# Optimization experiments

Hardware: AMD Instinct MI355X
Metric: run time of the kernel (lower is better)

The kernel has to match this reference:

```python
import jax, jax.numpy as jnp
import numpy as np
import math

N, E, LAT, MUL, HD = 20000, 160000, 128, 16, 32
H = LAT // HD          # 4 heads
D = 9                  # 0e+1o+2e spherical harmonics dim
SLICES = ((0, 1), (1, 4), (4, 9))
TPD = MUL * len(SLICES)


def _mlp(x, W1, b1, W2, b2):
    return jnp.dot(jax.nn.silu(jnp.dot(x, W1) + b1), W2) + b2


def _eq_linear(x, W):
    # block-diagonal per-l channel mixing: x [E, mul, D], W [n_l, mul, mul]
    return jnp.concatenate([jnp.einsum('ji,eim->ejm', W[l], x[:, :, s:t])
                            for l, (s, t) in enumerate(SLICES)], axis=-1)


def _residual(x, x_new, uc):
    co = jax.lax.rsqrt(uc * uc + 1.0)
    return co * x + (uc * co) * x_new


def _vec_rej(feat, dirs):
    d = dirs[:, None, :]
    return feat - (feat * d).sum(-1, keepdims=True) * d


def _so3_ln(x, eps=1e-8):
    # equivariant RMS layernorm per irrep block
    out = []
    for s, t in SLICES:
        blk = x[:, :, s:t]
        rms = jnp.sqrt((blk * blk).sum(-1).mean(-1) + eps)  # [N]
        out.append(blk / rms[:, None, None])
    return jnp.concatenate(out, axis=-1)


def _ln(x, g, b, eps=1e-5):
    mu = x.mean(-1, keepdims=True)
    var = ((x - mu) ** 2).mean(-1, keepdims=True)
    return (x - mu) * jax.lax.rsqrt(var + eps) * g + b


def _forward(h, X, t_ij, spharms, update_coeff, Wtq, Wtk, Wrs_W, Wrs_b, Wq_W, Wq_b, Wk_W, Wk_b, Wre_W, ln_g, ln_b, Wvu,
             gs_W1, gs_b1, gs_W2, gs_b2, gv_W1, gv_b1, gv_W2, gv_b2, gw_W1, gw_b1, gw_W2, gw_b2,
             gt_W1, gt_b1, gt_W2, gt_b2, gsp_W1, gsp_b1, gsp_W2, gsp_b2, md_W1, md_b1, md_W2, md_b2,
             mt_W1, mt_b1, mt_W2, mt_b2, gm_W1, gm_b1, gm_W2, gm_b2,
             edge_center, edge_neighbor, num_nodes):
    uc = update_coeff
    Xn = X[edge_neighbor]                                     # [E, mul, D]
    Xq = _vec_rej(_eq_linear(X[edge_center], Wtq), spharms)
    Xk = _vec_rej(_eq_linear(Xn, Wtk), -spharms)
    # CG scalar contraction (l x l -> 0e, uuu): normalized per-l dot product
    w = jnp.concatenate([(Xq[:, :, s:t] * Xk[:, :, s:t]).sum(-1) / math.sqrt(t - s)
                         for s, t in SLICES], axis=-1)        # [E, 3*mul]
    dt = _mlp(w, gw_W1, gw_b1, gw_W2, gw_b2) * _mlp(t_ij, gt_W1, gt_b1, gt_W2, gt_b2)
    t_ij = _residual(t_ij, dt, uc)
    h_i = h[edge_center]
    h_j = h[edge_neighbor]
    spatial = (t_ij @ Wrs_W + Wrs_b) * _mlp(h_j, gs_W1, gs_b1, gs_W2, gs_b2)
    En = t_ij.shape[0]
    q = (h_i @ Wq_W + Wq_b).reshape(En, H, HD)
    k = (h_j @ Wk_W + Wk_b).reshape(En, H, HD)
    v = _mlp(h_j, gv_W1, gv_b1, gv_W2, gv_b2)
    ta = jax.nn.silu(t_ij @ Wre_W).reshape(En, H, HD)
    alpha = (q * k * ta).sum(-1) / math.sqrt(HD)              # [E, H]
    amax = jax.ops.segment_max(alpha, edge_center, num_segments=num_nodes)
    ex = jnp.exp(alpha - amax[edge_center])
    den = jax.ops.segment_sum(ex, edge_center, num_segments=num_nodes)
    attn = ex / den[edge_center]                              # scatter_softmax
    sea = (attn[:, :, None] * v.reshape(En, H, HD)).reshape(En, LAT)
    combined = sea + spatial
    gates = _mlp(combined, gsp_W1, gsp_b1, gsp_W2, gsp_b2)
    o_s, o_d, o_t = gates[:, :LAT], gates[:, LAT:2 * LAT], gates[:, 2 * LAT:]
    dh = _ln(jax.ops.segment_sum(o_s, edge_center, num_segments=num_nodes), ln_g, ln_b)
    h = _residual(h, dh, uc)
    gd = _mlp(o_d, md_W1, md_b1, md_W2, md_b2)
    gtt = _mlp(o_t, mt_W1, mt_b1, mt_W2, mt_b2)
    dXij = gd[:, :, None] * spharms[:, None, :] + gtt[:, :, None] * Xn
    dX = _so3_ln(jax.ops.segment_sum(dXij, edge_center, num_segments=num_nodes))
    X = _residual(X, dX, uc)
    # EQFF
    Xp = jnp.einsum('nmi,mj->nji', X, Wvu)
    nrm = jnp.sqrt((Xp * Xp).sum(-1) + 1e-12)
    g = _mlp(jnp.concatenate([h, nrm], axis=-1), gm_W1, gm_b1, gm_W2, gm_b2)
    h = h + g[:, :LAT]
    X = X + g[:, LAT:, None] * Xp
    return h, X, t_ij


def setup_inputs() -> dict:
    key = jax.random.key(0)
    ks = jax.random.split(key, 24)

    def mk_mlp(k, din, dout):
        k1, k2 = jax.random.split(k)
        return (jax.random.normal(k1, (din, LAT)) / math.sqrt(din), jnp.zeros((LAT,)),
                jax.random.normal(k2, (LAT, dout)) / math.sqrt(LAT), jnp.zeros((dout,)))

    inp = {
        'h': jax.random.normal(ks[0], (N, LAT)),
        'X': jax.random.normal(ks[1], (N, MUL, D)),
        't_ij': jax.random.normal(ks[2], (E, LAT)),
        'spharms': jax.random.normal(ks[3], (E, D)),
        'update_coeff': jnp.ones((1,), dtype=jnp.float32),
        'Wtq': jax.random.normal(ks[4], (len(SLICES), MUL, MUL)) / math.sqrt(MUL),
        'Wtk': jax.random.normal(ks[5], (len(SLICES), MUL, MUL)) / math.sqrt(MUL),
        'Wrs_W': jax.random.normal(ks[6], (LAT, LAT)) / math.sqrt(LAT),
        'Wrs_b': jnp.zeros((LAT,)),
        'Wq_W': jax.random.normal(ks[7], (LAT, LAT)) / math.sqrt(LAT),
        'Wq_b': jnp.zeros((LAT,)),
        'Wk_W': jax.random.normal(ks[8], (LAT, LAT)) / math.sqrt(LAT),
        'Wk_b': jnp.zeros((LAT,)),
        'Wre_W': jax.random.normal(ks[9], (LAT, LAT)) / math.sqrt(LAT),
        'ln_g': jnp.ones((LAT,)),
        'ln_b': jnp.zeros((LAT,)),
        'Wvu': jax.random.normal(ks[10], (MUL, MUL)) / math.sqrt(MUL),
    }
    for name, din, dout, k in [('gs', LAT, LAT, ks[11]), ('gv', LAT, LAT, ks[12]), ('gw', TPD, LAT, ks[13]),
                               ('gt', LAT, LAT, ks[14]), ('gsp', LAT, 3 * LAT, ks[15]), ('md', LAT, MUL, ks[16]),
                               ('mt', LAT, MUL, ks[17]), ('gm', LAT + MUL, LAT + MUL, ks[18])]:
        W1, b1, W2, b2 = mk_mlp(k, din, dout)
        inp[name + '_W1'], inp[name + '_b1'], inp[name + '_W2'], inp[name + '_b2'] = W1, b1, W2, b2
    inp['edge_center'] = jax.random.randint(ks[19], (E,), 0, N)
    inp['edge_neighbor'] = jax.random.randint(ks[20], (E,), 0, N)
    inp['num_nodes'] = N
    return inp


def reference(h, X, t_ij, spharms, update_coeff, Wtq, Wtk, Wrs_W, Wrs_b, Wq_W, Wq_b, Wk_W, Wk_b, Wre_W, ln_g, ln_b, Wvu,
              gs_W1, gs_b1, gs_W2, gs_b2, gv_W1, gv_b1, gv_W2, gv_b2, gw_W1, gw_b1, gw_W2, gw_b2,
              gt_W1, gt_b1, gt_W2, gt_b2, gsp_W1, gsp_b1, gsp_W2, gsp_b2, md_W1, md_b1, md_W2, md_b2,
              mt_W1, mt_b1, mt_W2, mt_b2, gm_W1, gm_b1, gm_W2, gm_b2,
              edge_center, edge_neighbor, num_nodes):
    return _forward(h, X, t_ij, spharms, update_coeff, Wtq, Wtk, Wrs_W, Wrs_b, Wq_W, Wq_b, Wk_W, Wk_b, Wre_W, ln_g, ln_b, Wvu,
                    gs_W1, gs_b1, gs_W2, gs_b2, gv_W1, gv_b1, gv_W2, gv_b2, gw_W1, gw_b1, gw_W2, gw_b2,
                    gt_W1, gt_b1, gt_W2, gt_b2, gsp_W1, gsp_b1, gsp_W2, gsp_b2, md_W1, md_b1, md_W2, md_b2,
                    mt_W1, mt_b1, mt_W2, mt_b2, gm_W1, gm_b1, gm_W2, gm_b2,
                    edge_center, edge_neighbor, num_nodes)
```

## Files before the change

### kernel.cpp

```cpp
#include <hip/hip_runtime.h>
#include <math.h>

#define N_NODES 20000
#define E_EDGES 160000
#define LAT 128
#define MUL 16
#define DD 9
#define TPD 48

#define WS_QB     ((size_t)0)
#define WS_KB     (WS_QB + (size_t)N_NODES*LAT/2)
#define WS_VB     (WS_KB + (size_t)N_NODES*LAT/2)
#define WS_SB     (WS_VB + (size_t)N_NODES*LAT/2)
#define WS_W48    (WS_SB + (size_t)N_NODES*LAT/2)
#define WS_SPATB  (WS_W48 + (size_t)E_EDGES*TPD)
#define WS_ALPHA  (WS_SPATB + (size_t)E_EDGES*LAT/2)
#define WS_ZERO   (WS_ALPHA + (size_t)E_EDGES*4)
#define WS_AMAX   WS_ZERO
#define WS_DEN    (WS_AMAX + (size_t)N_NODES*4)
#define WS_HSUM   (WS_DEN + (size_t)N_NODES*4)
#define WS_NDX    (WS_HSUM + (size_t)N_NODES*LAT/2)
#define WS_END    (WS_NDX + (size_t)N_NODES*72)
#define ZERO_CNT  (WS_END - WS_ZERO)
#define WS_WB     WS_END

#define WOFF_WQ   0
#define WOFF_WK   16384
#define WOFF_GV1  32768
#define WOFF_GV2  49152
#define WOFF_GS1  65536
#define WOFF_GS2  81920
#define WOFF_GW1  98304
#define WOFF_GW2  106496
#define WOFF_GT1  122880
#define WOFF_GT2  139264
#define WOFF_WRS  155648
#define WOFF_WRE  172032
#define WOFF_GSP1 188416
#define WOFF_GSP2 204800
#define WOFF_MD1  253952
#define WOFF_MD2  270336
#define WOFF_MT1  272384
#define WOFF_MT2  288768
#define WB_TOTAL  290816

#define DEVI __device__ __forceinline__

typedef short short8 __attribute__((ext_vector_type(8)));
typedef float f32x4 __attribute__((ext_vector_type(4)));

DEVI float silu_f(float x){ return x / (1.f + __expf(-x)); }
DEVI unsigned int fmap(float x){ unsigned int b=__float_as_uint(x); return (b&0x80000000u)? ~b : (b|0x80000000u); }
DEVI float funmap(unsigned int u){ return (u&0x80000000u)? __uint_as_float(u&0x7fffffffu) : __uint_as_float(~u); }

DEVI unsigned short f2b(float f){ unsigned int u=__float_as_uint(f); return (unsigned short)((u + 0x7fffu + ((u>>16)&1u))>>16); }
DEVI unsigned int f2b2(float lo, float hi){ return ((unsigned int)f2b(hi)<<16) | (unsigned int)f2b(lo); }
DEVI float b2f(unsigned short u){ return __uint_as_float(((unsigned int)u)<<16); }

DEVI void atom_pk(unsigned short* p, unsigned int pk){
  asm volatile("global_atomic_pk_add_bf16 %0, %1, off" :: "v"(p), "v"(pk) : "memory");
}

DEVI f32x4 mfma16(short8 a, short8 b, f32x4 c){
  return __builtin_amdgcn_mfma_f32_16x16x32_bf16(a,b,c,0,0,0);
}

template<int KB>
DEVI void mm_tile2(const unsigned short* act, int strideUS, const unsigned short* Wp,
                   int ntile, int m, int quad, f32x4* acc){
  const unsigned short* wp = Wp + (size_t)ntile*KB*512 + (size_t)quad*128 + m*8;
  const unsigned short* a0 = act + m*strideUS + quad*8;
  const unsigned short* a1 = a0 + 16*strideUS;
  #pragma unroll
  for (int kb=0;kb<KB;++kb){
    short8 bfr = *(const short8*)(wp + (size_t)kb*512);
    short8 af0 = *(const short8*)(a0 + kb*32);
    short8 af1 = *(const short8*)(a1 + kb*32);
    acc[0]=mfma16(af0,bfr,acc[0]);
    acc[1]=mfma16(af1,bfr,acc[1]);
  }
}

template<int KB>
DEVI void mm_tile1(const unsigned short* act, int strideUS, const unsigned short* Wp,
                   int mtbase, int m, int quad, f32x4& acc){
  const unsigned short* wp = Wp + (size_t)quad*128 + m*8;
  const unsigned short* a0 = act + (mtbase*16+m)*strideUS + quad*8;
  #pragma unroll
  for (int kb=0;kb<KB;++kb){
    short8 bfr = *(const short8*)(wp + (size_t)kb*512);
    short8 af  = *(const short8*)(a0 + kb*32);
    acc=mfma16(af,bfr,acc);
  }
}

template<int R, int KD, int LDSTRIDE>
DEVI void mm_acc(const float* src, const float* __restrict__ W, int wstride, int t, float* acc){
  #pragma unroll 2
  for (int k=0;k<KD;k+=4){
    float4 xv[R];
    #pragma unroll
    for (int r=0;r<R;++r) xv[r] = *(const float4*)(src + r*LDSTRIDE + k);
    #pragma unroll
    for (int kk=0;kk<4;++kk){
      float wk = W[(size_t)(k+kk)*wstride + t];
      #pragma unroll
      for (int r=0;r<R;++r) acc[r] += ((const float*)&xv[r])[kk]*wk;
    }
  }
}

__global__ void k0_zero(float* __restrict__ z){
  size_t i = (size_t)blockIdx.x*256 + threadIdx.x;
  if (i < ZERO_CNT) z[i] = 0.f;
}

__global__ __launch_bounds__(256) void k_pack(
  const float* __restrict__ Wq,const float* __restrict__ Wk,
  const float* __restrict__ gv1,const float* __restrict__ gv2,
  const float* __restrict__ gs1,const float* __restrict__ gs2,
  const float* __restrict__ gw1,const float* __restrict__ gw2,
  const float* __restrict__ gt1,const float* __restrict__ gt2,
  const float* __restrict__ Wrs,const float* __restrict__ Wre,
  const float* __restrict__ gsp1,const float* __restrict__ gsp2,
  const float* __restrict__ md1,const float* __restrict__ md2,
  const float* __restrict__ mt1,const float* __restrict__ mt2,
  unsigned short* __restrict__ dst)
{
  int i = blockIdx.x*256 + threadIdx.x;
  if (i >= WB_TOTAL) return;
  const int off[19] = {0,16384,32768,49152,65536,81920,98304,106496,122880,139264,
                       155648,172032,188416,204800,253952,270336,272384,288768,290816};
  int mi=0;
  while (i >= off[mi+1]) ++mi;
  int li = i - off[mi];
  int N = (mi==13)?384:((mi==15||mi==17)?16:128);
  int Ksrc = (mi==6)?48:128;
  int KB = (mi==6)?2:4;
  int j = li&7; int t = li>>3;
  int n_in = t&15; t>>=4;
  int quad = t&3; t>>=2;
  int k_block = t % KB; int n_tile = t / KB;
  int k = k_block*32 + quad*8 + j;
  int n = n_tile*16 + n_in;
  const float* src;
  switch(mi){
    case 0: src=Wq; break;  case 1: src=Wk; break;
    case 2: src=gv1; break; case 3: src=gv2; break;
    case 4: src=gs1; break; case 5: src=gs2; break;
    case 6: src=gw1; break; case 7: src=gw2; break;
    case 8: src=gt1; break; case 9: src=gt2; break;
    case 10: src=Wrs; break; case 11: src=Wre; break;
    case 12: src=gsp1; break; case 13: src=gsp2; break;
    case 14: src=md1; break; case 15: src=md2; break;
    default: src=(mi==16)?mt1:mt2; break;
  }
  float v = (k < Ksrc) ? src[(size_t)k*N + n] : 0.f;
  dst[i] = f2b(v);
}

__global__ __launch_bounds__(256) void k1_node(const float* __restrict__ h,
  const unsigned short* __restrict__ WB,
  const float* __restrict__ Wq_b,const float* __restrict__ Wk_b,
  const float* __restrict__ gv_b1,const float* __restrict__ gv_b2,
  const float* __restrict__ gs_b1,const float* __restrict__ gs_b2,
  float* __restrict__ ws)
{
  __shared__ __align__(16) unsigned short B0[32*136], B1[32*136];
  const int tid=threadIdx.x, lane=tid&63, w=tid>>6, m=lane&15, quad=lane>>4;
  const int n0=blockIdx.x*32;
  for (int idx=tid; idx<1024; idx+=256){ int r=idx>>5, c4=(idx&31)*4;
    float4 hv = *(const float4*)(h+(size_t)(n0+r)*128+c4);
    *(unsigned int*)(B0+r*136+c4)   = f2b2(hv.x,hv.y);
    *(unsigned int*)(B0+r*136+c4+2) = f2b2(hv.z,hv.w); }
  __syncthreads();
  unsigned short* Qb=(unsigned short*)(ws+WS_QB);
  unsigned short* Kb=(unsigned short*)(ws+WS_KB);
  unsigned short* Vb=(unsigned short*)(ws+WS_VB);
  unsigned short* Sb=(unsigned short*)(ws+WS_SB);
  f32x4 z4 = {0.f,0.f,0.f,0.f};
  { f32x4 acc[2][2]={{z4,z4},{z4,z4}};
    #pragma unroll
    for(int i=0;i<2;++i) mm_tile2<4>(B0,136,WB+WOFF_WQ, w*2+i, m, quad, acc[i]);
    #pragma unroll
    for(int i=0;i<2;++i){ int col=(w*2+i)*16+m; float bv=Wq_b[col];
      #pragma unroll
      for(int mt=0;mt<2;++mt)
        #pragma unroll
        for(int r=0;r<4;++r){ int row=mt*16+quad*4+r;
          Qb[(size_t)(n0+row)*128+col]=f2b(acc[i][mt][r]+bv); } } }
  { f32x4 acc[2][2]={{z4,z4},{z4,z4}};
    #pragma unroll
    for(int i=0;i<2;++i) mm_tile2<4>(B0,136,WB+WOFF_WK, w*2+i, m, quad, acc[i]);
    #pragma unroll
    for(int i=0;i<2;++i){ int col=(w*2+i)*16+m; float bv=Wk_b[col];
      #pragma unroll
      for(int mt=0;mt<2;++mt)
        #pragma unroll
        for(int r=0;r<4;++r){ int row=mt*16+quad*4+r;
          Kb[(size_t)(n0+row)*128+col]=f2b(acc[i][mt][r]+bv); } } }
  { f32x4 acc[2][2]={{z4,z4},{z4,z4}};
    #pragma unroll
    for(int i=0;i<2;++i) mm_tile2<4>(B0,136,WB+WOFF_GV1, w*2+i, m, quad, acc[i]);
    #pragma unroll
    for(int i=0;i<2;++i){ int col=(w*2+i)*16+m; float bv=gv_b1[col];
      #pragma unroll
      for(int mt=0;mt<2;++mt)
        #pragma unroll
        for(int r=0;r<4;++r) B1[(mt*16+quad*4+r)*136+col]=f2b(silu_f(acc[i][mt][r]+bv)); } }
  __syncthreads();
  { f32x4 acc[2][2]={{z4,z4},{z4,z4}};
    #pragma unroll
    for(int i=0;i<2;++i) mm_tile2<4>(B1,136,WB+WOFF_GV2, w*2+i, m, quad, acc[i]);
    #pragma unroll
    for(int i=0;i<2;++i){ int col=(w*2+i)*16+m; float bv=gv_b2[col];
      #pragma unroll
      for(int mt=0;mt<2;++mt)
        #pragma unroll
        for(int r=0;r<4;++r){ int row=mt*16+quad*4+r;
          Vb[(size_t)(n0+row)*128+col]=f2b(acc[i][mt][r]+bv); } } }
  __syncthreads();
  { f32x4 acc[2][2]={{z4,z4},{z4,z4}};
    #pragma unroll
    for(int i=0;i<2;++i) mm_tile2<4>(B0,136,WB+WOFF_GS1, w*2+i, m, quad, acc[i]);
    #pragma unroll
    for(int i=0;i<2;++i){ int col=(w*2+i)*16+m; float bv=gs_b1[col];
      #pragma unroll
      for(int mt=0;mt<2;++mt)
        #pragma unroll
        for(int r=0;r<4;++r) B1[(mt*16+quad*4+r)*136+col]=f2b(silu_f(acc[i][mt][r]+bv)); } }
  __syncthreads();
  { f32x4 acc[2][2]={{z4,z4},{z4,z4}};
    #pragma unroll
    for(int i=0;i<2;++i) mm_tile2<4>(B1,136,WB+WOFF_GS2, w*2+i, m, quad, acc[i]);
    #pragma unroll
    for(int i=0;i<2;++i){ int col=(w*2+i)*16+m; float bv=gs_b2[col];
      #pragma unroll
      for(int mt=0;mt<2;++mt)
        #pragma unroll
        for(int r=0;r<4;++r){ int row=mt*16+quad*4+r;
          Sb[(size_t)(n0+row)*128+col]=f2b(acc[i][mt][r]+bv); } } }
}

__global__ __launch_bounds__(256) void k2_edge_w(
  const float* __restrict__ Xin, const float* __restrict__ sph,
  const float* __restrict__ Wtq, const float* __restrict__ Wtk,
  const int* __restrict__ ec, const int* __restrict__ en, float* __restrict__ ws)
{
  __shared__ float xc[16][144], xn[16][144], sphL[16][9];
  __shared__ float wq[768], wkk[768];
  __shared__ int ceI[16], nbI[16];
  const int tid=threadIdx.x, e0=blockIdx.x*16;
  if (tid<16){ ceI[tid]=ec[e0+tid]; nbI[tid]=en[e0+tid]; }
  for (int idx=tid; idx<768; idx+=256){ wq[idx]=Wtq[idx]; wkk[idx]=Wtk[idx]; }
  __syncthreads();
  for (int idx=tid; idx<2304; idx+=256){ int r=idx/144,c=idx%144;
    xc[r][c]=Xin[(size_t)ceI[r]*144+c]; xn[r][c]=Xin[(size_t)nbI[r]*144+c]; }
  if (tid<144){ int r=tid/9,c=tid%9; sphL[r][c]=sph[(size_t)(e0+r)*9+c]; }
  __syncthreads();
  const int el=tid>>4, j=tid&15;
  float xq[9], xk[9];
  const int ss[3]={0,1,4}, se[3]={1,4,9};
  #pragma unroll
  for (int l=0;l<3;++l){
    for (int mm2=ss[l]; mm2<se[l]; ++mm2){
      float aq=0.f, ak=0.f;
      #pragma unroll
      for (int i=0;i<16;++i){
        float wql = wq[l*256 + j*16 + i], wkl = wkk[l*256 + j*16 + i];
        aq += wql*xc[el][i*9+mm2];
        ak += wkl*xn[el][i*9+mm2];
      }
      xq[mm2]=aq; xk[mm2]=ak;
    }
  }
  float dq=0.f, dk=0.f;
  #pragma unroll
  for (int d=0; d<9; ++d){ dq += xq[d]*sphL[el][d]; dk += xk[d]*sphL[el][d]; }
  #pragma unroll
  for (int d=0; d<9; ++d){ xq[d] -= dq*sphL[el][d]; xk[d] -= dk*sphL[el][d]; }
  const float isc[3] = {1.f, 0.5773502691896258f, 0.4472135954999579f};
  unsigned short* W48u = (unsigned short*)(ws+WS_W48);
  #pragma unroll
  for (int l=0;l<3;++l){
    float s=0.f;
    for (int mm2=ss[l]; mm2<se[l]; ++mm2) s += xq[mm2]*xk[mm2];
    W48u[(size_t)(e0+el)*TPD + l*16 + j] = f2b(s*isc[l]);
  }
}

__global__ __launch_bounds__(256) void k3_edge_t(
  const float* __restrict__ t_in, const int* __restrict__ ec, const int* __restrict__ en,
  const unsigned short* __restrict__ WB,
  const float* __restrict__ gw_b1,const float* __restrict__ gw_b2,
  const float* __restrict__ gt_b1,const float* __restrict__ gt_b2,
  const float* __restrict__ Wrs_b,
  const float* __restrict__ ucp, float* __restrict__ ws, float* __restrict__ outT)
{
  __shared__ __align__(16) unsigned short tin_b[32*136], hid_b[32*136];
  __shared__ int ceI[32], nbI[32];
  const int tid=threadIdx.x, lane=tid&63, w=tid>>6, m=lane&15, quad=lane>>4;
  const int e0=blockIdx.x*32;
  if (tid<32){ ceI[tid]=ec[e0+tid]; nbI[tid]=en[e0+tid]; }
  for (int idx=tid; idx<1024; idx+=256){ int r=idx>>5, c4=(idx&31)*4;
    float4 tv = *(const float4*)(t_in+(size_t)(e0+r)*128+c4);
    *(unsigned int*)(tin_b+r*136+c4)   = f2b2(tv.x,tv.y);
    *(unsigned int*)(tin_b+r*136+c4+2) = f2b2(tv.z,tv.w); }
  const unsigned short* W48u=(const unsigned short*)(ws+WS_W48);
  short8 wfr[2][2];
  #pragma unroll
  for (int rr=0;rr<2;++rr){
    const unsigned short* base = W48u + (size_t)(e0 + rr*16 + m)*TPD;
    wfr[rr][0] = *(const short8*)(base + quad*8);
    if (quad<2) wfr[rr][1] = *(const short8*)(base + 32 + quad*8);
    else { short8 z = {0,0,0,0,0,0,0,0}; wfr[rr][1] = z; }
  }
  __syncthreads();
  const float uc=ucp[0], co=rsqrtf(uc*uc+1.f), ucco=uc*co;
  f32x4 z4 = {0.f,0.f,0.f,0.f};
  { f32x4 acc[2][2]={{z4,z4},{z4,z4}};
    #pragma unroll
    for(int i=0;i<2;++i){
      const unsigned short* wp = WB+WOFF_GW1 + (size_t)(w*2+i)*1024 + (size_t)quad*128 + m*8;
      #pragma unroll
      for(int kb=0;kb<2;++kb){
        short8 bfr = *(const short8*)(wp + (size_t)kb*512);
        acc[i][0]=mfma16(wfr[0][kb],bfr,acc[i][0]);
        acc[i][1]=mfma16(wfr[1][kb],bfr,acc[i][1]);
      }
    }
    #pragma unroll
    for(int i=0;i<2;++i){ int col=(w*2+i)*16+m; float bv=gw_b1[col];
      #pragma unroll
      for(int mt=0;mt<2;++mt)
        #pragma unroll
        for(int r=0;r<4;++r) hid_b[(mt*16+quad*4+r)*136+col]=f2b(silu_f(acc[i][mt][r]+bv)); } }
  __syncthreads();
  f32x4 accw[2][2]={{z4,z4},{z4,z4}};
  #pragma unroll
  for(int i=0;i<2;++i) mm_tile2<4>(hid_b,136,WB+WOFF_GW2, w*2+i, m, quad, accw[i]);
// ... 25 lines not shown
  unsigned short* spatB = (unsigned short*)(ws+WS_SPATB);
  const unsigned short* Sb=(const unsigned short*)(ws+WS_SB);
  { f32x4 acc[2][2]={{z4,z4},{z4,z4}};
    #pragma unroll
    for(int i=0;i<2;++i) mm_tile2<4>(tin_b,136,WB+WOFF_WRS, w*2+i, m, quad, acc[i]);
    #pragma unroll
    for(int i=0;i<2;++i){ int col=(w*2+i)*16+m; float bv=Wrs_b[col];
      #pragma unroll
      for(int mt=0;mt<2;++mt)
        #pragma unroll
        for(int r=0;r<4;++r){ int row=mt*16+quad*4+r;
          float sv=b2f(Sb[(size_t)nbI[row]*128+col]);
          spatB[(size_t)(e0+row)*128+col]=f2b((acc[i][mt][r]+bv)*sv); } } }
  { f32x4 acc[2][2]={{z4,z4},{z4,z4}};
    #pragma unroll
    for(int i=0;i<2;++i) mm_tile2<4>(tin_b,136,WB+WOFF_WRE, w*2+i, m, quad, acc[i]);
    const unsigned short* Qb=(const unsigned short*)(ws+WS_QB);
    const unsigned short* Kb=(const unsigned short*)(ws+WS_KB);
    unsigned int* amaxu=(unsigned int*)(ws+WS_AMAX);
    #pragma unroll
    for(int mt=0;mt<2;++mt)
      #pragma unroll
      for(int r=0;r<4;++r){ int row=mt*16+quad*4+r;
        int ce=ceI[row], nb=nbI[row];
        float p=0.f;
        #pragma unroll
        for(int i=0;i<2;++i){ int col=(w*2+i)*16+m;
          float qv=b2f(Qb[(size_t)ce*128+col]);
          float kv=b2f(Kb[(size_t)nb*128+col]);
          p += qv*kv*silu_f(acc[i][mt][r]); }
        p += __shfl_xor(p,1); p += __shfl_xor(p,2); p += __shfl_xor(p,4); p += __shfl_xor(p,8);
        if (m==0){
          float aval = p * 0.17677669529663687f;
          int e=e0+row;
          ws[WS_ALPHA+(size_t)e*4+w]=aval;
          atomicMax(&amaxu[(size_t)ce*4+w], fmap(aval));
        } } }
}

__global__ __launch_bounds__(256) void k4_softmax(const int* __restrict__ ec, float* __restrict__ ws){
  int i = blockIdx.x*256 + threadIdx.x;
  if (i >= E_EDGES*4) return;
  int e = i>>2, hh = i&3;
  int c = ec[e];
  float a = ws[WS_ALPHA + i];
  const unsigned int* amaxu = (const unsigned int*)(ws + WS_AMAX);
  float am = funmap(amaxu[(size_t)c*4+hh]);
  float exv = __expf(a - am);
  ws[WS_ALPHA + i] = exv;
  atomicAdd(&ws[WS_DEN + (size_t)c*4 + hh], exv);
}

__global__ __launch_bounds__(256) void k5_edge_gate(
  const float* __restrict__ Xin, const float* __restrict__ sph,
  const int* __restrict__ ec, const int* __restrict__ en,
  const unsigned short* __restrict__ WB,
  const float* __restrict__ gsp_b1,const float* __restrict__ gsp_b2,
  const float* __restrict__ md_b1,const float* __restrict__ md_b2,
  const float* __restrict__ mt_b1,const float* __restrict__ mt_b2,
  float* __restrict__ ws)
{
  __shared__ __align__(16) unsigned short A[32*136], B[32*136], C[32*136];
  __shared__ float gdL[32*16], gtL[32*16], attnL[32*4];
  __shared__ int ceI[32], nbI[32];
  const int tid=threadIdx.x, lane=tid&63, w=tid>>6, m=lane&15, quad=lane>>4;
  const int e0=blockIdx.x*32;
  if (tid<32){ ceI[tid]=ec[e0+tid]; nbI[tid]=en[e0+tid]; }
  __syncthreads();
  if (tid<128){ int r=tid>>2, hh=tid&3;
    attnL[tid] = ws[WS_ALPHA+(size_t)(e0+r)*4+hh] / ws[WS_DEN+(size_t)ceI[r]*4+hh]; }
  __syncthreads();
  const unsigned short* Vb=(const unsigned short*)(ws+WS_VB);
  const unsigned short* spatB=(const unsigned short*)(ws+WS_SPATB);
  for (int idx=tid; idx<2048; idx+=256){ int r=idx>>6, c2=(idx&63)*2;
    unsigned int va = *(const unsigned int*)(Vb+(size_t)nbI[r]*128+c2);
    unsigned int sp = *(const unsigned int*)(spatB+(size_t)(e0+r)*128+c2);
    float a = attnL[r*4+(c2>>5)];
    float v0 = a*b2f((unsigned short)va) + b2f((unsigned short)sp);
    float v1 = a*b2f((unsigned short)(va>>16)) + b2f((unsigned short)(sp>>16));
    *(unsigned int*)(A+r*136+c2) = f2b2(v0,v1); }
  __syncthreads();
  f32x4 z4 = {0.f,0.f,0.f,0.f};
  { f32x4 acc[2][2]={{z4,z4},{z4,z4}};
    #pragma unroll
    for(int i=0;i<2;++i) mm_tile2<4>(A,136,WB+WOFF_GSP1, w*2+i, m, quad, acc[i]);
    #pragma unroll
    for(int i=0;i<2;++i){ int col=(w*2+i)*16+m; float bv=gsp_b1[col];
      #pragma unroll
      for(int mt=0;mt<2;++mt)
        #pragma unroll
        for(int r=0;r<4;++r) B[(mt*16+quad*4+r)*136+col]=f2b(silu_f(acc[i][mt][r]+bv)); } }
  __syncthreads();
  { f32x4 acc[3][2][2];
    #pragma unroll
    for(int g2=0;g2<3;++g2)
      #pragma unroll
      for(int i=0;i<2;++i){ acc[g2][i][0]=z4; acc[g2][i][1]=z4; }
    #pragma unroll
    for(int g2=0;g2<3;++g2)
      #pragma unroll
      for(int i=0;i<2;++i)
        mm_tile2<4>(B,136,WB+WOFF_GSP2, g2*8+w*2+i, m, quad, acc[g2][i]);
    unsigned short* hsumB=(unsigned short*)(ws+WS_HSUM);
    #pragma unroll
    for(int i=0;i<2;++i){ int col=(w*2+i)*16+m;
      float bS=gsp_b2[col], bD=gsp_b2[128+col], bT=gsp_b2[256+col];
      #pragma unroll
      for(int mt=0;mt<2;++mt)
        #pragma unroll
        for(int r=0;r<4;++r){ int row=mt*16+quad*4+r;
          float vS = acc[0][i][mt][r]+bS;
          float vO = __shfl_xor(vS,1);
          if(!(m&1)){
            atom_pk(hsumB + (size_t)ceI[row]*128 + col, f2b2(vS,vO));
          }
          A[row*136+col]=f2b(acc[1][i][mt][r]+bD);
          C[row*136+col]=f2b(acc[2][i][mt][r]+bT); } } }
  __syncthreads();
  { f32x4 acc[2][2]={{z4,z4},{z4,z4}};
    #pragma unroll
    for(int i=0;i<2;++i) mm_tile2<4>(A,136,WB+WOFF_MD1, w*2+i, m, quad, acc[i]);
    #pragma unroll
    for(int i=0;i<2;++i){ int col=(w*2+i)*16+m; float bv=md_b1[col];
      #pragma unroll
      for(int mt=0;mt<2;++mt)
        #pragma unroll
        for(int r=0;r<4;++r) B[(mt*16+quad*4+r)*136+col]=f2b(silu_f(acc[i][mt][r]+bv)); } }
  __syncthreads();
  { f32x4 acc[2][2]={{z4,z4},{z4,z4}};
    #pragma unroll
    for(int i=0;i<2;++i) mm_tile2<4>(C,136,WB+WOFF_MT1, w*2+i, m, quad, acc[i]);
    #pragma unroll
    for(int i=0;i<2;++i){ int col=(w*2+i)*16+m; float bv=mt_b1[col];
      #pragma unroll
      for(int mt=0;mt<2;++mt)
        #pragma unroll
        for(int r=0;r<4;++r) A[(mt*16+quad*4+r)*136+col]=f2b(silu_f(acc[i][mt][r]+bv)); } }
  __syncthreads();
  { if (w<2){
      f32x4 a=z4; mm_tile1<4>(B,136,WB+WOFF_MD2, w, m, quad, a);
      #pragma unroll
      for(int r=0;r<4;++r) gdL[(w*16+quad*4+r)*16+m]=a[r]+md_b2[m];
    } else {
      f32x4 a=z4; mm_tile1<4>(A,136,WB+WOFF_MT2, w-2, m, quad, a);
      #pragma unroll
      for(int r=0;r<4;++r) gtL[((w-2)*16+quad*4+r)*16+m]=a[r]+mt_b2[m];
    } }
  __syncthreads();
  unsigned short* ndxB=(unsigned short*)(ws+WS_NDX);
  for (int idx=tid; idx<2304; idx+=256){
    int r=idx/72, p=idx-r*72; int c0=2*p, c1=c0+1;
    int mm0=c0/9, d0=c0-mm0*9;
    int mm1=c1/9, d1=c1-mm1*9;
    const float* sphE = sph + (size_t)(e0+r)*9;
    const float* xrow = Xin + (size_t)nbI[r]*144;
    float2 xv = *(const float2*)(xrow+c0);
    float v0 = gdL[r*16+mm0]*sphE[d0] + gtL[r*16+mm0]*xv.x;
    float v1 = gdL[r*16+mm1]*sphE[d1] + gtL[r*16+mm1]*xv.y;
    atom_pk(ndxB + (size_t)ceI[r]*144 + c0, f2b2(v0,v1));
  }
}

__global__ __launch_bounds__(128) void k6_node(
  const float* __restrict__ h, const float* __restrict__ Xin,
  const float* __restrict__ ln_g,const float* __restrict__ ln_b,
  const float* __restrict__ Wvu,
  const float* __restrict__ gm_W1,const float* __restrict__ gm_b1,
  const float* __restrict__ gm_W2,const float* __restrict__ gm_b2,
  const float* __restrict__ ucp, const float* __restrict__ ws,
  float* __restrict__ outH, float* __restrict__ outX)
{
  __shared__ float cat[4][144], dxb[4][144], xnw[4][144], xp[4][144], hid[4][LAT];
  __shared__ float red[4][2][2], rinv[4][3], gX[4][16], wvu[256];
  const int t=threadIdx.x, n0=blockIdx.x*4;
  const unsigned short* hsumB=(const unsigned short*)(ws+WS_HSUM);
  const unsigned short* ndxB =(const unsigned short*)(ws+WS_NDX);
  const float uc=ucp[0], co=rsqrtf(uc*uc+1.f), ucco=uc*co;
  for (int idx=t; idx<256; idx+=128) wvu[idx]=Wvu[idx];
  for (int idx=t; idx<576; idx+=128){ int r=idx/144,c=idx%144; dxb[r][c]=b2f(ndxB[(size_t)(n0+r)*144+c]); }
  float xv_[4];
  #pragma unroll
  for (int r=0;r<4;++r){
    float x=b2f(hsumB[(size_t)(n0+r)*LAT+t]); xv_[r]=x;
    float s=x, ss=x*x;
    for (int off=32; off; off>>=1){ s+=__shfl_down(s,off,64); ss+=__shfl_down(ss,off,64); }
    if ((t&63)==0){ red[r][t>>6][0]=s; red[r][t>>6][1]=ss; }
  }
  __syncthreads();
  #pragma unroll
  for (int r=0;r<4;++r){
    float s=red[r][0][0]+red[r][1][0], ss=red[r][0][1]+red[r][1][1];
    float mu=s*(1.f/128.f), var=ss*(1.f/128.f)-mu*mu;
    float dh=(xv_[r]-mu)*rsqrtf(var+1e-5f)*ln_g[t]+ln_b[t];
    cat[r][t]=co*h[(size_t)(n0+r)*LAT+t]+ucco*dh;
  }
  if (t<12){
    int r=t/3, l=t-r*3;
    int s0 = (l==0)?0:((l==1)?1:4);
    int s1 = (l==0)?1:((l==1)?4:9);
    float sum=0.f;
    for (int mm2=0;mm2<16;++mm2)
      for (int d=s0;d<s1;++d){ float v=dxb[r][mm2*9+d]; sum+=v*v; }
    rinv[r][l]=rsqrtf(sum*(1.f/16.f)+1e-8f);
  }
  __syncthreads();
  for (int idx=t; idx<144; idx+=128){
    int d=idx%9; int l=(d==0)?0:((d<4)?1:2);
    #pragma unroll
    for (int r=0;r<4;++r)
      xnw[r][idx]=co*Xin[(size_t)(n0+r)*144+idx]+ucco*dxb[r][idx]*rinv[r][l];
  }
// ... 41 lines not shown
    #pragma unroll
    for (int r=0;r<4;++r)
      outX[(size_t)(n0+r)*144+idx]=xnw[r][idx]+gX[r][j]*xp[r][idx];
  }
}

extern "C" void kernel_launch(void* const* d_in, const int* in_sizes, int n_in,
                              void* d_out, int out_size, void* d_ws, size_t ws_size,
                              hipStream_t stream)
{
  const float* h      = (const float*)d_in[0];
  const float* X      = (const float*)d_in[1];
  const float* t_ij   = (const float*)d_in[2];
  const float* sph    = (const float*)d_in[3];
  const float* ucp    = (const float*)d_in[4];
  const float* Wtq    = (const float*)d_in[5];
  const float* Wtk    = (const float*)d_in[6];
  const float* Wrs_W  = (const float*)d_in[7];
  const float* Wrs_b  = (const float*)d_in[8];
  const float* Wq_W   = (const float*)d_in[9];
  const float* Wq_b   = (const float*)d_in[10];
  const float* Wk_W   = (const float*)d_in[11];
  const float* Wk_b   = (const float*)d_in[12];
  const float* Wre_W  = (const float*)d_in[13];
  const float* ln_g   = (const float*)d_in[14];
  const float* ln_b   = (const float*)d_in[15];
  const float* Wvu    = (const float*)d_in[16];
  const float* gs_W1=(const float*)d_in[17], *gs_b1=(const float*)d_in[18],
             *gs_W2=(const float*)d_in[19], *gs_b2=(const float*)d_in[20];
  const float* gv_W1=(const float*)d_in[21], *gv_b1=(const float*)d_in[22],
             *gv_W2=(const float*)d_in[23], *gv_b2=(const float*)d_in[24];
  const float* gw_W1=(const float*)d_in[25], *gw_b1=(const float*)d_in[26],
             *gw_W2=(const float*)d_in[27], *gw_b2=(const float*)d_in[28];
  const float* gt_W1=(const float*)d_in[29], *gt_b1=(const float*)d_in[30],
             *gt_W2=(const float*)d_in[31], *gt_b2=(const float*)d_in[32];
  const float* gsp_W1=(const float*)d_in[33], *gsp_b1=(const float*)d_in[34],
             *gsp_W2=(const float*)d_in[35], *gsp_b2=(const float*)d_in[36];
  const float* md_W1=(const float*)d_in[37], *md_b1=(const float*)d_in[38],
             *md_W2=(const float*)d_in[39], *md_b2=(const float*)d_in[40];
  const float* mt_W1=(const float*)d_in[41], *mt_b1=(const float*)d_in[42],
             *mt_W2=(const float*)d_in[43], *mt_b2=(const float*)d_in[44];
  const float* gm_W1=(const float*)d_in[45], *gm_b1=(const float*)d_in[46],
             *gm_W2=(const float*)d_in[47], *gm_b2=(const float*)d_in[48];
  const int* ec = (const int*)d_in[49];
  const int* en = (const int*)d_in[50];
  (void)in_sizes; (void)n_in; (void)out_size; (void)ws_size;

  float* ws   = (float*)d_ws;
  unsigned short* WB = (unsigned short*)(ws + WS_WB);
  float* outH = (float*)d_out;
  float* outX = outH + (size_t)N_NODES*LAT;
  float* outT = outX + (size_t)N_NODES*MUL*DD;

  k0_zero<<<dim3((unsigned)((ZERO_CNT+255)/256)), dim3(256), 0, stream>>>(ws + WS_ZERO);
  k_pack<<<dim3((WB_TOTAL+255)/256), dim3(256), 0, stream>>>(
      Wq_W,Wk_W, gv_W1,gv_W2, gs_W1,gs_W2, gw_W1,gw_W2, gt_W1,gt_W2,
      Wrs_W,Wre_W, gsp_W1,gsp_W2, md_W1,md_W2, mt_W1,mt_W2, WB);
  k1_node<<<dim3(N_NODES/32), dim3(256), 0, stream>>>(h, WB, Wq_b, Wk_b,
      gv_b1,gv_b2, gs_b1,gs_b2, ws);
  k2_edge_w<<<dim3(E_EDGES/16), dim3(256), 0, stream>>>(X, sph, Wtq, Wtk, ec, en, ws);
  k3_edge_t<<<dim3(E_EDGES/32), dim3(256), 0, stream>>>(t_ij, ec, en, WB,
      gw_b1,gw_b2, gt_b1,gt_b2, Wrs_b, ucp, ws, outT);
  k4_softmax<<<dim3((E_EDGES*4)/256), dim3(256), 0, stream>>>(ec, ws);
  k5_edge_gate<<<dim3(E_EDGES/32), dim3(256), 0, stream>>>(X, sph, ec, en, WB,
      gsp_b1,gsp_b2, md_b1,md_b2, mt_b1,mt_b2, ws);
  k6_node<<<dim3(N_NODES/4), dim3(128), 0, stream>>>(h, X, ln_g, ln_b, Wvu,
      gm_W1,gm_b1,gm_W2,gm_b2, ucp, ws, outH, outX);
}
```

Before: 782.8 us.

## Merge prep kernels, fuse node and edge-w kernels, gather X in bf16

Combines the zero-fill and weight-pack kernels into one prep launch, which also converts X to bf16 in the workspace. The node projection kernel and the edge w-contraction kernel now run as one launch, split by block index, so they can overlap instead of executing back to back. Edge gathers of X in the edge-w and gate kernels read the bf16 copy, halving the bytes gathered per edge. The cost is reduced precision on X in those paths and an extra pass over X to convert it.

Measured after the change: 897.7 us. 1.15x slower.

```diff
diff --git a/kernel.cpp b/kernel.cpp
--- a/kernel.cpp
+++ b/kernel.cpp
@@ -23,6 +23,7 @@
 #define WS_END    (WS_NDX + (size_t)N_NODES*72)
 #define ZERO_CNT  (WS_END - WS_ZERO)
 #define WS_WB     WS_END
+#define WS_XB     (WS_WB + (size_t)145408)
 
 #define WOFF_WQ   0
 #define WOFF_WK   16384
@@ -44,6 +45,12 @@
 #define WOFF_MT2  288768
 #define WB_TOTAL  290816
 
+#define PREP_ZB   11250
+#define PREP_PB   1136
+#define PREP_XB   5625
+#define K1B       (N_NODES/32)
+#define K2B       (E_EDGES/16)
+
 #define DEVI __device__ __forceinline__
 
 typedef short short8 __attribute__((ext_vector_type(8)));
@@ -110,12 +117,8 @@
   }
 }
 
-__global__ void k0_zero(float* __restrict__ z){
-  size_t i = (size_t)blockIdx.x*256 + threadIdx.x;
-  if (i < ZERO_CNT) z[i] = 0.f;
-}
-
-__global__ __launch_bounds__(256) void k_pack(
+__global__ __launch_bounds__(256) void k_prep(
+  const float* __restrict__ X,
   const float* __restrict__ Wq,const float* __restrict__ Wk,
   const float* __restrict__ gv1,const float* __restrict__ gv2,
   const float* __restrict__ gs1,const float* __restrict__ gs2,
@@ -125,167 +128,196 @@
   const float* __restrict__ gsp1,const float* __restrict__ gsp2,
   const float* __restrict__ md1,const float* __restrict__ md2,
   const float* __restrict__ mt1,const float* __restrict__ mt2,
-  unsigned short* __restrict__ dst)
+  float* __restrict__ ws)
 {
-  int i = blockIdx.x*256 + threadIdx.x;
-  if (i >= WB_TOTAL) return;
-  const int off[19] = {0,16384,32768,49152,65536,81920,98304,106496,122880,139264,
-                       155648,172032,188416,204800,253952,270336,272384,288768,290816};
-  int mi=0;
-  while (i >= off[mi+1]) ++mi;
-  int li = i - off[mi];
-  int N = (mi==13)?384:((mi==15||mi==17)?16:128);
-  int Ksrc = (mi==6)?48:128;
-  int KB = (mi==6)?2:4;
-  int j = li&7; int t = li>>3;
-  int n_in = t&15; t>>=4;
-  int quad = t&3; t>>=2;
-  int k_block = t % KB; int n_tile = t / KB;
-  int k = k_block*32 + quad*8 + j;
-  int n = n_tile*16 + n_in;
-  const float* src;
-  switch(mi){
-    case 0: src=Wq; break;  case 1: src=Wk; break;
-    case 2: src=gv1; break; case 3: src=gv2; break;
-    case 4: src=gs1; break; case 5: src=gs2; break;
-    case 6: src=gw1; break; case 7: src=gw2; break;
-    case 8: src=gt1; break; case 9: src=gt2; break;
-    case 10: src=Wrs; break; case 11: src=Wre; break;
-    case 12: src=gsp1; break; case 13: src=gsp2; break;
-    case 14: src=md1; break; case 15: src=md2; break;
-    default: src=(mi==16)?mt1:mt2; break;
-  }
-  float v = (k < Ksrc) ? src[(size_t)k*N + n] : 0.f;
-  dst[i] = f2b(v);
-}
-
-__global__ __launch_bounds__(256) void k1_node(const float* __restrict__ h,
+  const int b = blockIdx.x, tid = threadIdx.x;
+  if (b < PREP_ZB){
+    size_t i = (size_t)b*256 + tid;
+    if (i < ZERO_CNT) ws[WS_ZERO + i] = 0.f;
+    return;
+  }
+  if (b < PREP_ZB + PREP_PB){
+    int i = (b - PREP_ZB)*256 + tid;
+    if (i >= WB_TOTAL) return;
+    unsigned short* dst = (unsigned short*)(ws + WS_WB);
+    const int off[19] = {0,16384,32768,49152,65536,81920,98304,106496,122880,139264,
+                         155648,172032,188416,204800,253952,270336,272384,288768,290816};
+    int mi=0;
+    while (i >= off[mi+1]) ++mi;
+    int li = i - off[mi];
+    int N = (mi==13)?384:((mi==15||mi==17)?16:128);
+    int Ksrc = (mi==6)?48:128;
+    int KB = (mi==6)?2:4;
+    int j = li&7; int t = li>>3;
+    int n_in = t&15; t>>=4;
+    int quad = t&3; t>>=2;
+    int k_block = t % KB; int n_tile = t / KB;
+    int k = k_block*32 + quad*8 + j;
+    int n = n_tile*16 + n_in;
+    const float* src;
+    switch(mi){
+      case 0: src=Wq; break;  case 1: src=Wk; break;
+      case 2: src=gv1; break; case 3: src=gv2; break;
+      case 4: src=gs1; break; case 5: src=gs2; break;
+      case 6: src=gw1; break; case 7: src=gw2; break;
+      case 8: src=gt1; break; case 9: src=gt2; break;
+      case 10: src=Wrs; break; case 11: src=Wre; break;
+      case 12: src=gsp1; break; case 13: src=gsp2; break;
+      case 14: src=md1; break; case 15: src=md2; break;
+      default: src=(mi==16)?mt1:mt2; break;
+    }
+    float v = (k < Ksrc) ? src[(size_t)k*N + n] : 0.f;
+    dst[i] = f2b(v);
+    return;
+  }
+  {
+    size_t idx = (size_t)(b - PREP_ZB - PREP_PB)*256 + tid;
+    if (idx < (size_t)N_NODES*72){
+      float2 v = *(const float2*)(X + idx*2);
+      ((unsigned int*)(ws + WS_XB))[idx] = f2b2(v.x, v.y);
+    }
+    return;
+  }
+}
+
+__global__ __launch_bounds__(256) void k12_node_edge(
+  const float* __restrict__ h, const float* __restrict__ sph,
+  const float* __restrict__ Wtq, const float* __restrict__ Wtk,
+  const int* __restrict__ ec, const int* __restrict__ en,
   const unsigned short* __restrict__ WB,
   const float* __restrict__ Wq_b,const float* __restrict__ Wk_b,
   const float* __restrict__ gv_b1,const float* __restrict__ gv_b2,
   const float* __restrict__ gs_b1,const float* __restrict__ gs_b2,
   float* __restrict__ ws)
 {
-  __shared__ __align__(16) unsigned short B0[32*136], B1[32*136];
-  const int tid=threadIdx.x, lane=tid&63, w=tid>>6, m=lane&15, quad=lane>>4;
-  const int n0=blockIdx.x*32;
-  for (int idx=tid; idx<1024; idx+=256){ int r=idx>>5, c4=(idx&31)*4;
-    float4 hv = *(const float4*)(h+(size_t)(n0+r)*128+c4);
-    *(unsigned int*)(B0+r*136+c4)   = f2b2(hv.x,hv.y);
-    *(unsigned int*)(B0+r*136+c4+2) = f2b2(hv.z,hv.w); }
-  __syncthreads();
-  unsigned short* Qb=(unsigned short*)(ws+WS_QB);
-  unsigned short* Kb=(unsigned short*)(ws+WS_KB);
-  unsigned short* Vb=(unsigned short*)(ws+WS_VB);
-  unsigned short* Sb=(unsigned short*)(ws+WS_SB);
-  f32x4 z4 = {0.f,0.f,0.f,0.f};
-  { f32x4 acc[2][2]={{z4,z4},{z4,z4}};
-    #pragma unroll
-    for(int i=0;i<2;++i) mm_tile2<4>(B0,136,WB+WOFF_WQ, w*2+i, m, quad, acc[i]);
-    #pragma unroll
-    for(int i=0;i<2;++i){ int col=(w*2+i)*16+m; float bv=Wq_b[col];
-      #pragma unroll
-      for(int mt=0;mt<2;++mt)
-        #pragma unroll
-        for(int r=0;r<4;++r){ int row=mt*16+quad*4+r;
-          Qb[(size_t)(n0+row)*128+col]=f2b(acc[i][mt][r]+bv); } } }
-  { f32x4 acc[2][2]={{z4,z4},{z4,z4}};
-    #pragma unroll
-    for(int i=0;i<2;++i) mm_tile2<4>(B0,136,WB+WOFF_WK, w*2+i, m, quad, acc[i]);
-    #pragma unroll
-    for(int i=0;i<2;++i){ int col=(w*2+i)*16+m; float bv=Wk_b[col];
-      #pragma unroll
-      for(int mt=0;mt<2;++mt)
-        #pragma unroll
-        for(int r=0;r<4;++r){ int row=mt*16+quad*4+r;
-          Kb[(size_t)(n0+row)*128+col]=f2b(acc[i][mt][r]+bv); } } }
-  { f32x4 acc[2][2]={{z4,z4},{z4,z4}};
-    #pragma unroll
-    for(int i=0;i<2;++i) mm_tile2<4>(B0,136,WB+WOFF_GV1, w*2+i, m, quad, acc[i]);
-    #pragma unroll
-    for(int i=0;i<2;++i){ int col=(w*2+i)*16+m; float bv=gv_b1[col];
-      #pragma unroll
-      for(int mt=0;mt<2;++mt)
-        #pragma unroll
-        for(int r=0;r<4;++r) B1[(mt*16+quad*4+r)*136+col]=f2b(silu_f(acc[i][mt][r]+bv)); } }
-  __syncthreads();
-  { f32x4 acc[2][2]={{z4,z4},{z4,z4}};
-    #pragma unroll
-    for(int i=0;i<2;++i) mm_tile2<4>(B1,136,WB+WOFF_GV2, w*2+i, m, quad, acc[i]);
-    #pragma unroll
-    for(int i=0;i<2;++i){ int col=(w*2+i)*16+m; float bv=gv_b2[col];
-      #pragma unroll
-      for(int mt=0;mt<2;++mt)
-        #pragma unroll
-        for(int r=0;r<4;++r){ int row=mt*16+quad*4+r;
-          Vb[(size_t)(n0+row)*128+col]=f2b(acc[i][mt][r]+bv); } } }
-  __syncthreads();
-  { f32x4 acc[2][2]={{z4,z4},{z4,z4}};
-    #pragma unroll
-    for(int i=0;i<2;++i) mm_tile2<4>(B0,136,WB+WOFF_GS1, w*2+i, m, quad, acc[i]);
-    #pragma unroll
-    for(int i=0;i<2;++i){ int col=(w*2+i)*16+m; float bv=gs_b1[col];
-      #pragma unroll
-      for(int mt=0;mt<2;++mt)
-        #pragma unroll
-        for(int r=0;r<4;++r) B1[(mt*16+quad*4+r)*136+col]=f2b(silu_f(acc[i][mt][r]+bv)); } }
-  __syncthreads();
-  { f32x4 acc[2][2]={{z4,z4},{z4,z4}};
-    #pragma unroll
-    for(int i=0;i<2;++i) mm_tile2<4>(B1,136,WB+WOFF_GS2, w*2+i, m, quad, acc[i]);
-    #pragma unroll
-    for(int i=0;i<2;++i){ int col=(w*2+i)*16+m; float bv=gs_b2[col];
-      #pragma unroll
-      for(int mt=0;mt<2;++mt)
-        #pragma unroll
-        for(int r=0;r<4;++r){ int row=mt*16+quad*4+r;
-          Sb[(size_t)(n0+row)*128+col]=f2b(acc[i][mt][r]+bv); } } }
-}
-
-__global__ __launch_bounds__(256) void k2_edge_w(
-  const float* __restrict__ Xin, const float* __restrict__ sph,
-  const float* __restrict__ Wtq, const float* __restrict__ Wtk,
-  const int* __restrict__ ec, const int* __restrict__ en, float* __restrict__ ws)
-{
-  __shared__ float xc[16][144], xn[16][144], sphL[16][9];
-  __shared__ float wq[768], wkk[768];
-  __shared__ int ceI[16], nbI[16];
-  const int tid=threadIdx.x, e0=blockIdx.x*16;
-  if (tid<16){ ceI[tid]=ec[e0+tid]; nbI[tid]=en[e0+tid]; }
-  for (int idx=tid; idx<768; idx+=256){ wq[idx]=Wtq[idx]; wkk[idx]=Wtk[idx]; }
-  __syncthreads();
-  for (int idx=tid; idx<2304; idx+=256){ int r=idx/144,c=idx%144;
-    xc[r][c]=Xin[(size_t)ceI[r]*144+c]; xn[r][c]=Xin[(size_t)nbI[r]*144+c]; }
-  if (tid<144){ int r=tid/9,c=tid%9; sphL[r][c]=sph[(size_t)(e0+r)*9+c]; }
-  __syncthreads();
-  const int el=tid>>4, j=tid&15;
-  float xq[9], xk[9];
-  const int ss[3]={0,1,4}, se[3]={1,4,9};
-  #pragma unroll
-  for (int l=0;l<3;++l){
-    for (int mm2=ss[l]; mm2<se[l]; ++mm2){
-      float aq=0.f, ak=0.f;
-      #pragma unroll
-      for (int i=0;i<16;++i){
-        float wql = wq[l*256 + j*16 + i], wkl = wkk[l*256 + j*16 + i];
-        aq += wql*xc[el][i*9+mm2];
-        ak += wkl*xn[el][i*9+mm2];
+  __shared__ __align__(16) unsigned short SH[8704];
+  const int tid=threadIdx.x;
+  if (blockIdx.x < K1B){
+    unsigned short* B0 = SH;
+    unsigned short* B1 = SH + 32*136;
+    const int lane=tid&63, w=tid>>6, m=lane&15, quad=lane>>4;
+    const int n0=blockIdx.x*32;
+    for (int idx=tid; idx<1024; idx+=256){ int r=idx>>5, c4=(idx&31)*4;
+      float4 hv = *(const float4*)(h+(size_t)(n0+r)*128+c4);
+      *(unsigned int*)(B0+r*136+c4)   = f2b2(hv.x,hv.y);
+      *(unsigned int*)(B0+r*136+c4+2) = f2b2(hv.z,hv.w); }
+    __syncthreads();
+    unsigned short* Qb=(unsigned short*)(ws+WS_QB);
+    unsigned short* Kb=(unsigned short*)(ws+WS_KB);
+    unsigned short* Vb=(unsigned short*)(ws+WS_VB);
+    unsigned short* Sb=(unsigned short*)(ws+WS_SB);
+    f32x4 z4 = {0.f,0.f,0.f,0.f};
+    { f32x4 acc[2][2]={{z4,z4},{z4,z4}};
+      #pragma unroll
+      for(int i=0;i<2;++i) mm_tile2<4>(B0,136,WB+WOFF_WQ, w*2+i, m, quad, acc[i]);
+      #pragma unroll
+      for(int i=0;i<2;++i){ int col=(w*2+i)*16+m; float bv=Wq_b[col];
+        #pragma unroll
+        for(int mt=0;mt<2;++mt)
+          #pragma unroll
+          for(int r=0;r<4;++r){ int row=mt*16+quad*4+r;
+            Qb[(size_t)(n0+row)*128+col]=f2b(acc[i][mt][r]+bv); } } }
+    { f32x4 acc[2][2]={{z4,z4},{z4,z4}};
+      #pragma unroll
+      for(int i=0;i<2;++i) mm_tile2<4>(B0,136,WB+WOFF_WK, w*2+i, m, quad, acc[i]);
+      #pragma unroll
+      for(int i=0;i<2;++i){ int col=(w*2+i)*16+m; float bv=Wk_b[col];
+        #pragma unroll
+        for(int mt=0;mt<2;++mt)
+          #pragma unroll
+          for(int r=0;r<4;++r){ int row=mt*16+quad*4+r;
+            Kb[(size_t)(n0+row)*128+col]=f2b(acc[i][mt][r]+bv); } } }
+    { f32x4 acc[2][2]={{z4,z4},{z4,z4}};
+      #pragma unroll
+      for(int i=0;i<2;++i) mm_tile2<4>(B0,136,WB+WOFF_GV1, w*2+i, m, quad, acc[i]);
+      #pragma unroll
+      for(int i=0;i<2;++i){ int col=(w*2+i)*16+m; float bv=gv_b1[col];
+        #pragma unroll
+        for(int mt=0;mt<2;++mt)
+          #pragma unroll
+          for(int r=0;r<4;++r) B1[(mt*16+quad*4+r)*136+col]=f2b(silu_f(acc[i][mt][r]+bv)); } }
+    __syncthreads();
+    { f32x4 acc[2][2]={{z4,z4},{z4,z4}};
+      #pragma unroll
+      for(int i=0;i<2;++i) mm_tile2<4>(B1,136,WB+WOFF_GV2, w*2+i, m, quad, acc[i]);
+      #pragma unroll
+      for(int i=0;i<2;++i){ int col=(w*2+i)*16+m; float bv=gv_b2[col];
+        #pragma unroll
+        for(int mt=0;mt<2;++mt)
+          #pragma unroll
+          for(int r=0;r<4;++r){ int row=mt*16+quad*4+r;
+            Vb[(size_t)(n0+row)*128+col]=f2b(acc[i][mt][r]+bv); } } }
+    __syncthreads();
+    { f32x4 acc[2][2]={{z4,z4},{z4,z4}};
+      #pragma unroll
+      for(int i=0;i<2;++i) mm_tile2<4>(B0,136,WB+WOFF_GS1, w*2+i, m, quad, acc[i]);
+      #pragma unroll
+      for(int i=0;i<2;++i){ int col=(w*2+i)*16+m; float bv=gs_b1[col];
+        #pragma unroll
+        for(int mt=0;mt<2;++mt)
+          #pragma unroll
+          for(int r=0;r<4;++r) B1[(mt*16+quad*4+r)*136+col]=f2b(silu_f(acc[i][mt][r]+bv)); } }
+    __syncthreads();
+    { f32x4 acc[2][2]={{z4,z4},{z4,z4}};
+      #pragma unroll
+      for(int i=0;i<2;++i) mm_tile2<4>(B1,136,WB+WOFF_GS2, w*2+i, m, quad, acc[i]);
+      #pragma unroll
+      for(int i=0;i<2;++i){ int col=(w*2+i)*16+m; float bv=gs_b2[col];
+        #pragma unroll
+        for(int mt=0;mt<2;++mt)
+          #pragma unroll
+          for(int r=0;r<4;++r){ int row=mt*16+quad*4+r;
+            Sb[(size_t)(n0+row)*128+col]=f2b(acc[i][mt][r]+bv); } } }
+    return;
+  }
+  {
+    unsigned short* xcb = SH;
+    unsigned short* xnb = SH + 2304;
+    float* sphL = (float*)(SH + 4608);
+    float* wq   = (float*)(SH + 4896);
+    float* wkk  = (float*)(SH + 6432);
+    int*   ceI  = (int*)(SH + 7968);
+    int*   nbI  = (int*)(SH + 8032);
+    const int e0=(blockIdx.x - K1B)*16;
+    if (tid<16){ ceI[tid]=ec[e0+tid]; nbI[tid]=en[e0+tid]; }
+    for (int idx=tid; idx<768; idx+=256){ wq[idx]=Wtq[idx]; wkk[idx]=Wtk[idx]; }
+    __syncthreads();
+    const unsigned short* Xb=(const unsigned short*)(ws+WS_XB);
+    for (int idx=tid; idx<1152; idx+=256){ int r=idx/72, p=idx-r*72;
+      *(unsigned int*)(xcb + r*144 + 2*p) = *(const unsigned int*)(Xb + (size_t)ceI[r]*144 + 2*p);
+      *(unsigned int*)(xnb + r*144 + 2*p) = *(const unsigned int*)(Xb + (size_t)nbI[r]*144 + 2*p); }
+    if (tid<144){ int r=tid/9,c=tid%9; sphL[r*9+c]=sph[(size_t)(e0+r)*9+c]; }
+    __syncthreads();
+    const int el=tid>>4, j=tid&15;
+    float xq[9], xk[9];
+    const int ss[3]={0,1,4}, se[3]={1,4,9};
+    #pragma unroll
+    for (int l=0;l<3;++l){
+      for (int mm2=ss[l]; mm2<se[l]; ++mm2){
+        float aq=0.f, ak=0.f;
+        #pragma unroll
+        for (int i=0;i<16;++i){
+          float wql = wq[l*256 + j*16 + i], wkl = wkk[l*256 + j*16 + i];
+          aq += wql*b2f(xcb[el*144 + i*9+mm2]);
+          ak += wkl*b2f(xnb[el*144 + i*9+mm2]);
+        }
+        xq[mm2]=aq; xk[mm2]=ak;
       }
-      xq[mm2]=aq; xk[mm2]=ak;
     }
-  }
-  float dq=0.f, dk=0.f;
-  #pragma unroll
-  for (int d=0; d<9; ++d){ dq += xq[d]*sphL[el][d]; dk += xk[d]*sphL[el][d]; }
-  #pragma unroll
-  for (int d=0; d<9; ++d){ xq[d] -= dq*sphL[el][d]; xk[d] -= dk*sphL[el][d]; }
-  const float isc[3] = {1.f, 0.5773502691896258f, 0.4472135954999579f};
-  unsigned short* W48u = (unsigned short*)(ws+WS_W48);
-  #pragma unroll
-  for (int l=0;l<3;++l){
-    float s=0.f;
-    for (int mm2=ss[l]; mm2<se[l]; ++mm2) s += xq[mm2]*xk[mm2];
-    W48u[(size_t)(e0+el)*TPD + l*16 + j] = f2b(s*isc[l]);
+    float dq=0.f, dk=0.f;
+    #pragma unroll
+    for (int d=0; d<9; ++d){ dq += xq[d]*sphL[el*9+d]; dk += xk[d]*sphL[el*9+d]; }
+    #pragma unroll
+    for (int d=0; d<9; ++d){ xq[d] -= dq*sphL[el*9+d]; xk[d] -= dk*sphL[el*9+d]; }
+    const float isc[3] = {1.f, 0.5773502691896258f, 0.4472135954999579f};
+    unsigned short* W48u = (unsigned short*)(ws+WS_W48);
+    #pragma unroll
+    for (int l=0;l<3;++l){
+      float s=0.f;
+      for (int mm2=ss[l]; mm2<se[l]; ++mm2) s += xq[mm2]*xk[mm2];
+      W48u[(size_t)(e0+el)*TPD + l*16 + j] = f2b(s*isc[l]);
+    }
+    return;
   }
 }
 
@@ -417,7 +449,7 @@
 }
 
 __global__ __launch_bounds__(256) void k5_edge_gate(
-  const float* __restrict__ Xin, const float* __restrict__ sph,
+  const float* __restrict__ sph,
   const int* __restrict__ ec, const int* __restrict__ en,
   const unsigned short* __restrict__ WB,
   const float* __restrict__ gsp_b1,const float* __restrict__ gsp_b2,
@@ -513,15 +545,16 @@
     } }
   __syncthreads();
   unsigned short* ndxB=(unsigned short*)(ws+WS_NDX);
+  const unsigned short* Xb=(const unsigned short*)(ws+WS_XB);
   for (int idx=tid; idx<2304; idx+=256){
     int r=idx/72, p=idx-r*72; int c0=2*p, c1=c0+1;
     int mm0=c0/9, d0=c0-mm0*9;
     int mm1=c1/9, d1=c1-mm1*9;
     const float* sphE = sph + (size_t)(e0+r)*9;
-    const float* xrow = Xin + (size_t)nbI[r]*144;
-    float2 xv = *(const float2*)(xrow+c0);
-    float v0 = gdL[r*16+mm0]*sphE[d0] + gtL[r*16+mm0]*xv.x;
-    float v1 = gdL[r*16+mm1]*sphE[d1] + gtL[r*16+mm1]*xv.y;
+    unsigned int xa = *(const unsigned int*)(Xb + (size_t)nbI[r]*144 + c0);
+    float x0=b2f((unsigned short)xa), x1=b2f((unsigned short)(xa>>16));
+    float v0 = gdL[r*16+mm0]*sphE[d0] + gtL[r*16+mm0]*x0;
+    float v1 = gdL[r*16+mm1]*sphE[d1] + gtL[r*16+mm1]*x1;
     atom_pk(ndxB + (size_t)ceI[r]*144 + c0, f2b2(v0,v1));
   }
 }
@@ -669,17 +702,15 @@
   float* outX = outH + (size_t)N_NODES*LAT;
   float* outT = outX + (size_t)N_NODES*MUL*DD;
 
-  k0_zero<<<dim3((unsigned)((ZERO_CNT+255)/256)), dim3(256), 0, stream>>>(ws + WS_ZERO);
-  k_pack<<<dim3((WB_TOTAL+255)/256), dim3(256), 0, stream>>>(
-      Wq_W,Wk_W, gv_W1,gv_W2, gs_W1,gs_W2, gw_W1,gw_W2, gt_W1,gt_W2,
-      Wrs_W,Wre_W, gsp_W1,gsp_W2, md_W1,md_W2, mt_W1,mt_W2, WB);
-  k1_node<<<dim3(N_NODES/32), dim3(256), 0, stream>>>(h, WB, Wq_b, Wk_b,
-      gv_b1,gv_b2, gs_b1,gs_b2, ws);
-  k2_edge_w<<<dim3(E_EDGES/16), dim3(256), 0, stream>>>(X, sph, Wtq, Wtk, ec, en, ws);
+  k_prep<<<dim3(PREP_ZB + PREP_PB + PREP_XB), dim3(256), 0, stream>>>(
+      X, Wq_W,Wk_W, gv_W1,gv_W2, gs_W1,gs_W2, gw_W1,gw_W2, gt_W1,gt_W2,
+      Wrs_W,Wre_W, gsp_W1,gsp_W2, md_W1,md_W2, mt_W1,mt_W2, ws);
+  k12_node_edge<<<dim3(K1B + K2B), dim3(256), 0, stream>>>(
+      h, sph, Wtq, Wtk, ec, en, WB, Wq_b, Wk_b, gv_b1,gv_b2, gs_b1,gs_b2, ws);
   k3_edge_t<<<dim3(E_EDGES/32), dim3(256), 0, stream>>>(t_ij, ec, en, WB,
       gw_b1,gw_b2, gt_b1,gt_b2, Wrs_b, ucp, ws, outT);
   k4_softmax<<<dim3((E_EDGES*4)/256), dim3(256), 0, stream>>>(ec, ws);
-  k5_edge_gate<<<dim3(E_EDGES/32), dim3(256), 0, stream>>>(X, sph, ec, en, WB,
+  k5_edge_gate<<<dim3(E_EDGES/32), dim3(256), 0, stream>>>(sph, ec, en, WB,
       gsp_b1,gsp_b2, md_b1,md_b2, mt_b1,mt_b2, ws);
   k6_node<<<dim3(N_NODES/4), dim3(128), 0, stream>>>(h, X, ln_g, ln_b, Wvu,
       gm_W1,gm_b1,gm_W2,gm_b2, ucp, ws, outH, outX);
```
